# Kernel optimization log

Measured on AMD Instinct MI355X. Metric: run time of the kernel, lower is better.

## Reference

```python
import jax, jax.numpy as jnp
import numpy as np

B, T, D, H = 2, 4096, 768, 12
DK = D // H

def setup_inputs() -> dict:
    key = jax.random.key(0)
    ks = jax.random.split(key, 5)
    scale = 1.0 / np.sqrt(D)
    x = jax.random.normal(ks[0], (B, T, D), dtype=jnp.float32)
    WQ = jax.random.normal(ks[1], (D, D), dtype=jnp.float32) * scale
    WK = jax.random.normal(ks[2], (D, D), dtype=jnp.float32) * scale
    WV = jax.random.normal(ks[3], (D, D), dtype=jnp.float32) * scale
    Wproj = jax.random.normal(ks[4], (D, D), dtype=jnp.float32) * scale
    return {"x": x, "WQ": WQ, "WK": WK, "WV": WV, "Wproj": Wproj}

def reference(x, WQ, WK, WV, Wproj):
    # Weights stored as [in, out] (torch Linear weight transposed): y = x @ W
    def split_heads(y):
        return y.reshape(B, T, H, DK).transpose(0, 2, 1, 3)  # [B,H,T,DK]
    Q = split_heads(x @ WQ)
    K = split_heads(x @ WK)
    V = split_heads(x @ WV)
    score = jnp.einsum('bhqd,bhkd->bhqk', Q, K) * (DK ** -0.5)  # [B,H,T,T]
    attn = jax.nn.softmax(score, axis=-1)
    out = jnp.einsum('bhqk,bhkd->bhqd', attn, V)  # [B,H,T,DK]
    out = out.transpose(0, 2, 1, 3).reshape(B, T, D)
    return out @ Wproj
```

## Files before the change

kernel.cpp:

```cpp
#include <hip/hip_runtime.h>
#include <stdint.h>

#define B_ 2
#define T_ 4096
#define D_ 768
#define H_ 12
#define DK_ 64
#define BH_ 24

typedef unsigned short u16;
typedef unsigned int u32;
typedef __bf16 bf16x8 __attribute__((ext_vector_type(8)));
typedef float f32x4 __attribute__((ext_vector_type(4)));
typedef short s16x8 __attribute__((ext_vector_type(8)));

__device__ __forceinline__ float exp2_raw(float x) {
#if __has_builtin(__builtin_amdgcn_exp2f)
    return __builtin_amdgcn_exp2f(x);
#else
    float y; asm("v_exp_f32 %0, %1" : "=v"(y) : "v"(x)); return y;
#endif
}

__device__ __forceinline__ f32x4 mfma16(bf16x8 a, bf16x8 b, f32x4 c) {
    return __builtin_amdgcn_mfma_f32_16x16x32_bf16(a, b, c, 0, 0, 0);
}

__device__ __forceinline__ u16 f2bf(float f) {
    union { float f; u32 u; } v; v.f = f;
    u32 r = v.u + 0x7FFFu + ((v.u >> 16) & 1u);
    return (u16)(r >> 16);
}

__device__ __forceinline__ u32 pack2bf(float lo, float hi) {
    union { float f; u32 u; } a, b; a.f = lo; b.f = hi;
    return __builtin_amdgcn_perm(b.u + 0x8000u, a.u + 0x8000u, 0x07060302u);
}

__device__ __forceinline__ void gll16(const u16* g, u16* l) {
    __builtin_amdgcn_global_load_lds(
        (const __attribute__((address_space(1))) u32*)g,
        (__attribute__((address_space(3))) u32*)l, 16, 0, 0);
}

__global__ __launch_bounds__(256) void prep_kernel(
    const float* __restrict__ x,
    const float* __restrict__ w0, const float* __restrict__ w1,
    const float* __restrict__ w2, const float* __restrict__ w3,
    u16* __restrict__ xb, u16* __restrict__ wt)
{
    __shared__ u16 tile[32][33];
    int bid = blockIdx.x;
    if (bid < 3072) {
        int i = (bid * 256 + threadIdx.x) * 8;
        float4 a = *(const float4*)&x[i];
        float4 b = *(const float4*)&x[i + 4];
        uint4 dd;
        dd.x = pack2bf(a.x, a.y); dd.y = pack2bf(a.z, a.w);
        dd.z = pack2bf(b.x, b.y); dd.w = pack2bf(b.z, b.w);
        *(uint4*)&xb[i] = dd;
    } else {
        int id = bid - 3072;
        int z = id / 576;
        int rest = id % 576;
        int by = rest / 24, bx = rest % 24;
        const float* src = (z == 0) ? w0 : (z == 1) ? w1 : (z == 2) ? w2 : w3;
        u16* dst = wt + (size_t)z * D_ * D_;
        int tx = threadIdx.x & 31, ty = threadIdx.x >> 5;
        int x0 = bx * 32, y0 = by * 32;
        for (int i = ty; i < 32; i += 8) tile[i][tx] = f2bf(src[(size_t)(y0 + i) * D_ + x0 + tx]);
        __syncthreads();
        for (int i = ty; i < 32; i += 8) dst[(size_t)(x0 + i) * D_ + y0 + tx] = tile[tx][i];
    }
}

template<int MODE>
__global__ __launch_bounds__(256) void gemm_bt(
    const u16* __restrict__ A, const u16* __restrict__ Bt, void* __restrict__ outv)
{
    __shared__ u16 As[128 * 64];
    __shared__ u16 Bs[128 * 64];
    const int K = 768;
    int tid = threadIdx.x;
    int lane = tid & 63, wave = tid >> 6;
    int r = lane & 15, quad = lane >> 4;
    int rx = r & 7;
    int m0 = blockIdx.y * 128, n0 = blockIdx.x * 128;
    int wrow = (wave >> 1) * 64, wcol = (wave & 1) * 64;

    int srow = wave * 32 + (lane >> 3);
    int scol = ((lane & 7) ^ (lane >> 3)) * 8;
    const u16* Ag = A + (size_t)(m0 + srow) * K + scol;
    const u16* Bg = Bt + (size_t)(n0 + srow) * K + scol;

    f32x4 acc[4][4];
    #pragma unroll
    for (int i = 0; i < 4; i++)
        #pragma unroll
        for (int j = 0; j < 4; j++)
            #pragma unroll
            for (int e = 0; e < 4; e++) acc[i][j][e] = 0.f;

    for (int k0 = 0; k0 < K; k0 += 64) {
        __syncthreads();
        #pragma unroll
        for (int j = 0; j < 4; j++) {
            gll16(Ag + (size_t)j * 8 * K + k0, As + (wave * 32 + j * 8) * 64);
            gll16(Bg + (size_t)j * 8 * K + k0, Bs + (wave * 32 + j * 8) * 64);
        }
        __syncthreads();
        #pragma unroll
        for (int ks = 0; ks < 2; ks++) {
            int swz = ((ks * 4 + quad) ^ rx) * 8;
            bf16x8 af[4], bfr[4];
            #pragma unroll
            for (int mi = 0; mi < 4; mi++)
                af[mi] = *(const bf16x8*)&As[(wrow + mi * 16 + r) * 64 + swz];
            #pragma unroll
            for (int ni = 0; ni < 4; ni++)
                bfr[ni] = *(const bf16x8*)&Bs[(wcol + ni * 16 + r) * 64 + swz];
            #pragma unroll
            for (int mi = 0; mi < 4; mi++)
                #pragma unroll
                for (int ni = 0; ni < 4; ni++)
                    acc[mi][ni] = mfma16(af[mi], bfr[ni], acc[mi][ni]);
        }
    }

    if (MODE == 0) {
        u16* out = (u16*)outv;
        int which = n0 / D_;
        int nb = n0 % D_;
        const size_t HS = (size_t)B_ * H_ * T_ * DK_;
        if (which == 2) {
            u16* vt = out + 2 * HS;
            #pragma unroll
            for (int mi = 0; mi < 4; mi++) {
                int mg = m0 + wrow + mi * 16 + quad * 4;
                int b = mg >> 12, t = mg & 4095;
                #pragma unroll
                for (int ni = 0; ni < 4; ni++) {
                    int ng = nb + wcol + ni * 16 + r;
                    int h = ng >> 6, dk = ng & 63;
                    uint2 d;
                    d.x = pack2bf(acc[mi][ni][0], acc[mi][ni][1]);
                    d.y = pack2bf(acc[mi][ni][2], acc[mi][ni][3]);
                    *(uint2*)&vt[(((size_t)(b * H_ + h)) * DK_ + dk) * T_ + t] = d;
                }
            }
        } else {
            const float cf = (which == 0) ? 0.18033688011112042f : 1.0f;
            size_t wbase = (size_t)which * HS;
            #pragma unroll
            for (int mi = 0; mi < 4; mi++) {
                #pragma unroll
                for (int ni = 0; ni < 4; ni++) {
                    int ng = nb + wcol + ni * 16 + r;
                    int h = ng >> 6, dk = ng & 63;
                    #pragma unroll
                    for (int e = 0; e < 4; e++) {
                        int mg = m0 + wrow + mi * 16 + quad * 4 + e;
                        int b = mg >> 12, t = mg & 4095;
                        out[wbase + (((size_t)(b * H_ + h)) * T_ + t) * DK_ + dk]
                            = f2bf(acc[mi][ni][e] * cf);
                    }
                }
            }
        }
    } else {
        float* out = (float*)outv;
        #pragma unroll
        for (int mi = 0; mi < 4; mi++)
            #pragma unroll
            for (int ni = 0; ni < 4; ni++)
                #pragma unroll
                for (int e = 0; e < 4; e++)
                    out[(size_t)(m0 + wrow + mi * 16 + quad * 4 + e) * D_ + n0 + wcol + ni * 16 + r]
                        = acc[mi][ni][e];
    }
}

__global__ __launch_bounds__(512, 4) void attn_kernel(
    const u16* __restrict__ Q, const u16* __restrict__ K,
    const u16* __restrict__ VT, float* __restrict__ pO, float* __restrict__ pL)
{
    __shared__ u16 Ks[128 * 64];
    __shared__ u16 Vs[2][64 * 64];

    int tid = threadIdx.x;
    int lane = tid & 63, w = tid >> 6;
    int r = lane & 15, quad = lane >> 4;

    int wgid = blockIdx.x;
    int xcd = wgid & 7, slot = wgid >> 3;
    int bh = xcd * 3 + (slot >> 5);
    int rem = slot & 31;
    int z = rem >> 4;
    int q0 = (rem & 15) * 256;

    bf16x8 qf[2][2];
    #pragma unroll
    for (int qi = 0; qi < 2; qi++) {
        const u16* Qb = Q + ((size_t)bh * T_ + q0 + w * 32 + qi * 16 + r) * DK_;
        qf[qi][0] = *(const bf16x8*)(Qb + quad * 8);
        qf[qi][1] = *(const bf16x8*)(Qb + 32 + quad * 8);
    }

    bf16x8 ones;
    #pragma unroll
    for (int j = 0; j < 8; j++) ones[j] = (__bf16)1.0f;

    f32x4 fzero;
    #pragma unroll
    for (int e = 0; e < 4; e++) fzero[e] = 0.f;

    f32x4 o[2][4];
    f32x4 lacc[2];
    #pragma unroll
    for (int qi = 0; qi < 2; qi++) {
        #pragma unroll
        for (int e = 0; e < 4; e++) lacc[qi][e] = 0.f;
        #pragma unroll
        for (int n = 0; n < 4; n++)
            #pragma unroll
            for (int e = 0; e < 4; e++) o[qi][n][e] = 0.f;
    }

    int kb0 = z * (T_ / 2), kb1 = kb0 + T_ / 2;
    int rb = ((r >> 2) * 8) + (r & 3);

    int kls = lane >> 3;
    int sgcK1 = (lane & 7) ^ (kls & 3);
    const u16* KgA = K + ((size_t)bh * T_ + w * 16 + kls) * DK_ + sgcK1 * 8;
    const u16* KgB = K + ((size_t)bh * T_ + w * 16 + 8 + kls) * DK_ + (sgcK1 ^ 4) * 8;
    u16* KsA = &Ks[(w * 16) * 64];
    u16* KsB = &Ks[(w * 16 + 8) * 64];

    int srow = w * 8 + (lane >> 3);
    int sfr = (w & 1) * 4 + ((lane >> 3) & 3);
    int sgcV = (lane & 7) ^ sfr;
    const u16* Vg = VT + ((size_t)bh * DK_ + srow) * T_ + sgcV * 8;
    u16* Vs0Base = &Vs[0][(w * 8) * 64];
    u16* Vs1Base = &Vs[1][(w * 8) * 64];

    for (int kb = kb0; kb < kb1; kb += 128) {
        __syncthreads();
        gll16(KgA + (size_t)kb * DK_, KsA);
        gll16(KgB + (size_t)kb * DK_, KsB);
        gll16(Vg + kb, Vs0Base);
        gll16(Vg + kb + 64, Vs1Base);
        __syncthreads();

        #pragma unroll
        for (int s = 0; s < 4; s++) {
            int rowA = s * 32 + rb;
            int rowB = rowA + 4;
            int fA = ((rowA >> 3) & 1) * 4 + (rowA & 3);
            int fB = ((rowB >> 3) & 1) * 4 + (rowB & 3);
            bf16x8 kA0 = *(const bf16x8*)&Ks[rowA * 64 + (quad ^ fA) * 8];
            bf16x8 kA1 = *(const bf16x8*)&Ks[rowA * 64 + (((4 + quad) ^ fA)) * 8];
            bf16x8 kB0 = *(const bf16x8*)&Ks[rowB * 64 + (quad ^ fB) * 8];
            bf16x8 kB1 = *(const bf16x8*)&Ks[rowB * 64 + (((4 + quad) ^ fB)) * 8];
            const u16* Vsub = Vs[s >> 1];
            bf16x8 vf[4];
            #pragma unroll
            for (int ndk = 0; ndk < 4; ndk++) {
                int row = ndk * 16 + r;
                int fvr = ((row >> 3) & 1) * 4 + (row & 3);
                vf[ndk] = *(const bf16x8*)&Vsub[row * 64 + ((((s & 1) * 4 + quad) ^ fvr)) * 8];
            }
            #pragma unroll
            for (int qi = 0; qi < 2; qi++) {
                f32x4 zA, zB;
                zA = mfma16(kA0, qf[qi][0], fzero);
                zA = mfma16(kA1, qf[qi][1], zA);
                zB = mfma16(kB0, qf[qi][0], fzero);
                zB = mfma16(kB1, qf[qi][1], zB);
                bf16x8 pf;
                pf[0] = (__bf16)exp2_raw(zA[0]);
                pf[1] = (__bf16)exp2_raw(zA[1]);
                pf[2] = (__bf16)exp2_raw(zA[2]);
                pf[3] = (__bf16)exp2_raw(zA[3]);
                pf[4] = (__bf16)exp2_raw(zB[0]);
                pf[5] = (__bf16)exp2_raw(zB[1]);
                pf[6] = (__bf16)exp2_raw(zB[2]);
                pf[7] = (__bf16)exp2_raw(zB[3]);
                lacc[qi] = mfma16(ones, pf, lacc[qi]);
                #pragma unroll
                for (int ndk = 0; ndk < 4; ndk++)
                    o[qi][ndk] = mfma16(vf[ndk], pf, o[qi][ndk]);
            }
        }
    }

    const size_t SP = (size_t)BH_ * T_ * DK_;
    #pragma unroll
    for (int qi = 0; qi < 2; qi++) {
        int q = q0 + w * 32 + qi * 16 + r;
        float* base = pO + (size_t)z * SP + ((size_t)bh * T_ + q) * DK_;
        #pragma unroll
        for (int ndk = 0; ndk < 4; ndk++)
            *(f32x4*)&base[ndk * 16 + quad * 4] = o[qi][ndk];
    }
    if (quad == 0) {
        #pragma unroll
        for (int qi = 0; qi < 2; qi++)
            pL[(size_t)z * BH_ * T_ + (size_t)bh * T_ + q0 + w * 32 + qi * 16 + r]
                = lacc[qi][0];
    }
}

__global__ __launch_bounds__(256) void combine_kernel(
    const float* __restrict__ pO, const float* __restrict__ pL, u16* __restrict__ AO)
{
    const size_t SP = (size_t)BH_ * T_ * DK_;
    int bh = blockIdx.y;
    int b = bh / H_, h = bh % H_;
    int q = blockIdx.x * 64 + (threadIdx.x >> 2);
    int dk0 = (threadIdx.x & 3) * 16;
    size_t idx = ((size_t)bh * T_ + q) * DK_ + dk0;
    float l0 = pL[(size_t)bh * T_ + q];
    float l1 = pL[(size_t)BH_ * T_ + (size_t)bh * T_ + q];
    float inv = 1.0f / (l0 + l1);
    u16* dst = AO + ((size_t)b * T_ + q) * D_ + h * DK_ + dk0;
    #pragma unroll
    for (int i = 0; i < 2; i++) {
        float4 a0 = *(const float4*)&pO[idx + i * 8];
        float4 a1 = *(const float4*)&pO[idx + i * 8 + 4];
        float4 b0 = *(const float4*)&pO[SP + idx + i * 8];
        float4 b1 = *(const float4*)&pO[SP + idx + i * 8 + 4];
        uint4 dd;
        dd.x = pack2bf((a0.x + b0.x) * inv, (a0.y + b0.y) * inv);
        dd.y = pack2bf((a0.z + b0.z) * inv, (a0.w + b0.w) * inv);
        dd.z = pack2bf((a1.x + b1.x) * inv, (a1.y + b1.y) * inv);
        dd.w = pack2bf((a1.z + b1.z) * inv, (a1.w + b1.w) * inv);
        *(uint4*)&dst[i * 8] = dd;
    }
}

extern "C" void kernel_launch(void* const* d_in, const int* in_sizes, int n_in,
                              void* d_out, int out_size, void* d_ws, size_t ws_size,
                              hipStream_t stream)
{
    const float* x  = (const float*)d_in[0];
    const float* wq = (const float*)d_in[1];
    const float* wk = (const float*)d_in[2];
    const float* wv = (const float*)d_in[3];
    const float* wp = (const float*)d_in[4];

    u16* ws = (u16*)d_ws;
    const size_t XS = (size_t)B_ * T_ * D_;
    const size_t WT = (size_t)D_ * D_;
    const size_t HS = (size_t)B_ * H_ * T_ * DK_;
    u16* xb = ws;
    u16* wt = xb + XS;
    u16* q  = wt + 4 * WT;
    u16* k  = q + HS;
    u16* vt = k + HS;
    u16* ao = vt + HS;
    float* pL = (float*)(ao + HS);
    float* pO = pL + 2 * (size_t)BH_ * T_;

    prep_kernel<<<dim3(3072 + 2304), 256, 0, stream>>>(x, wq, wk, wv, wp, xb, wt);
    gemm_bt<0><<<dim3(18, 64), 256, 0, stream>>>(xb, wt, q);
    attn_kernel<<<dim3(768), 512, 0, stream>>>(q, k, vt, pO, pL);
    combine_kernel<<<dim3(64, 24), 256, 0, stream>>>(pO, pL, ao);
    gemm_bt<1><<<dim3(6, 64), 256, 0, stream>>>(ao, wt + 3 * WT, d_out);
}
```

Measured before the change: 257.2 us.

## Fuse split-KV combine into output projection GEMM A-tile loading

Removes the separate combine kernel. The output-projection GEMM now builds its A tile directly from the two fp32 partial attention outputs and their row sums, normalizes them, converts to bf16 and stores them into swizzled shared memory. This saves one launch plus the write and re-read of the bf16 attention-output buffer. In exchange, each of the 6 column blocks re-reads the fp32 partials, so that traffic is repeated sixfold. The A-side loads are also now synchronous global loads inside the K loop rather than async copies.

After: 284.9 us. 10.8% more time.

```diff
diff --git a/kernel.cpp b/kernel.cpp
--- a/kernel.cpp
+++ b/kernel.cpp
@@ -74,9 +74,8 @@
     }
 }
 
-template<int MODE>
 __global__ __launch_bounds__(256) void gemm_bt(
-    const u16* __restrict__ A, const u16* __restrict__ Bt, void* __restrict__ outv)
+    const u16* __restrict__ A, const u16* __restrict__ Bt, u16* __restrict__ out)
 {
     __shared__ u16 As[128 * 64];
     __shared__ u16 Bs[128 * 64];
@@ -127,8 +126,7 @@
         }
     }
 
-    if (MODE == 0) {
-        u16* out = (u16*)outv;
+    {
         int which = n0 / D_;
         int nb = n0 % D_;
         const size_t HS = (size_t)B_ * H_ * T_ * DK_;
@@ -167,17 +165,101 @@
                 }
             }
         }
-    } else {
-        float* out = (float*)outv;
-        #pragma unroll
-        for (int mi = 0; mi < 4; mi++)
+    }
+}
+
+__global__ __launch_bounds__(256) void gemm_combine(
+    const float* __restrict__ pO, const float* __restrict__ pL,
+    const u16* __restrict__ Bt, float* __restrict__ out)
+{
+    __shared__ u16 As[128 * 64];
+    __shared__ u16 Bs[128 * 64];
+    const int K = 768;
+    const size_t SP = (size_t)BH_ * T_ * DK_;
+    const size_t LP = (size_t)BH_ * T_;
+    int tid = threadIdx.x;
+    int lane = tid & 63, wave = tid >> 6;
+    int r = lane & 15, quad = lane >> 4;
+    int rx = r & 7;
+    int m0 = blockIdx.y * 128, n0 = blockIdx.x * 128;
+    int wrow = (wave >> 1) * 64, wcol = (wave & 1) * 64;
+
+    int srow = wave * 32 + (lane >> 3);
+    int scol = ((lane & 7) ^ (lane >> 3)) * 8;
+    const u16* Bg = Bt + (size_t)(n0 + srow) * K + scol;
+
+    size_t cO[4];
+    size_t cL[4];
+    #pragma unroll
+    for (int j = 0; j < 4; j++) {
+        int mg = m0 + srow + j * 8;
+        int b = mg >> 12, q = mg & 4095;
+        cO[j] = ((size_t)b * H_ * T_ + q) * DK_ + scol;
+        cL[j] = (size_t)b * H_ * T_ + q;
+    }
+    u16* AsW = As + (size_t)0;
+
+    f32x4 acc[4][4];
+    #pragma unroll
+    for (int i = 0; i < 4; i++)
+        #pragma unroll
+        for (int j = 0; j < 4; j++)
+            #pragma unroll
+            for (int e = 0; e < 4; e++) acc[i][j][e] = 0.f;
+
+    for (int k0 = 0; k0 < K; k0 += 64) {
+        int h = k0 >> 6;
+        size_t hO = (size_t)h * T_ * DK_;
+        size_t hL = (size_t)h * T_;
+        __syncthreads();
+        #pragma unroll
+        for (int j = 0; j < 4; j++)
+            gll16(Bg + (size_t)j * 8 * K + k0, Bs + (wave * 32 + j * 8) * 64);
+        #pragma unroll
+        for (int j = 0; j < 4; j++) {
+            float l0 = pL[cL[j] + hL];
+            float l1 = pL[LP + cL[j] + hL];
+            float inv = 1.0f / (l0 + l1);
+            const float* p0 = pO + cO[j] + hO;
+            const float* p1 = pO + SP + cO[j] + hO;
+            float4 a0 = *(const float4*)&p0[0];
+            float4 a1 = *(const float4*)&p0[4];
+            float4 b0 = *(const float4*)&p1[0];
+            float4 b1 = *(const float4*)&p1[4];
+            uint4 dd;
+            dd.x = pack2bf((a0.x + b0.x) * inv, (a0.y + b0.y) * inv);
+            dd.y = pack2bf((a0.z + b0.z) * inv, (a0.w + b0.w) * inv);
+            dd.z = pack2bf((a1.x + b1.x) * inv, (a1.y + b1.y) * inv);
+            dd.w = pack2bf((a1.z + b1.z) * inv, (a1.w + b1.w) * inv);
+            *(uint4*)&AsW[(wave * 32 + j * 8) * 64 + lane * 8] = dd;
+        }
+        __syncthreads();
+        #pragma unroll
+        for (int ks = 0; ks < 2; ks++) {
+            int swz = ((ks * 4 + quad) ^ rx) * 8;
+            bf16x8 af[4], bfr[4];
+            #pragma unroll
+            for (int mi = 0; mi < 4; mi++)
+                af[mi] = *(const bf16x8*)&As[(wrow + mi * 16 + r) * 64 + swz];
             #pragma unroll
             for (int ni = 0; ni < 4; ni++)
+                bfr[ni] = *(const bf16x8*)&Bs[(wcol + ni * 16 + r) * 64 + swz];
+            #pragma unroll
+            for (int mi = 0; mi < 4; mi++)
                 #pragma unroll
-                for (int e = 0; e < 4; e++)
-                    out[(size_t)(m0 + wrow + mi * 16 + quad * 4 + e) * D_ + n0 + wcol + ni * 16 + r]
-                        = acc[mi][ni][e];
-    }
+                for (int ni = 0; ni < 4; ni++)
+                    acc[mi][ni] = mfma16(af[mi], bfr[ni], acc[mi][ni]);
+        }
+    }
+
+    #pragma unroll
+    for (int mi = 0; mi < 4; mi++)
+        #pragma unroll
+        for (int ni = 0; ni < 4; ni++)
+            #pragma unroll
+            for (int e = 0; e < 4; e++)
+                out[(size_t)(m0 + wrow + mi * 16 + quad * 4 + e) * D_ + n0 + wcol + ni * 16 + r]
+                    = acc[mi][ni][e];
 }
 
 __global__ __launch_bounds__(512, 4) void attn_kernel(
@@ -310,34 +392,6 @@
     }
 }
 
-__global__ __launch_bounds__(256) void combine_kernel(
-    const float* __restrict__ pO, const float* __restrict__ pL, u16* __restrict__ AO)
-{
-    const size_t SP = (size_t)BH_ * T_ * DK_;
-    int bh = blockIdx.y;
-    int b = bh / H_, h = bh % H_;
-    int q = blockIdx.x * 64 + (threadIdx.x >> 2);
-    int dk0 = (threadIdx.x & 3) * 16;
-    size_t idx = ((size_t)bh * T_ + q) * DK_ + dk0;
-    float l0 = pL[(size_t)bh * T_ + q];
-    float l1 = pL[(size_t)BH_ * T_ + (size_t)bh * T_ + q];
-    float inv = 1.0f / (l0 + l1);
-    u16* dst = AO + ((size_t)b * T_ + q) * D_ + h * DK_ + dk0;
-    #pragma unroll
-    for (int i = 0; i < 2; i++) {
-        float4 a0 = *(const float4*)&pO[idx + i * 8];
-        float4 a1 = *(const float4*)&pO[idx + i * 8 + 4];
-        float4 b0 = *(const float4*)&pO[SP + idx + i * 8];
-        float4 b1 = *(const float4*)&pO[SP + idx + i * 8 + 4];
-        uint4 dd;
-        dd.x = pack2bf((a0.x + b0.x) * inv, (a0.y + b0.y) * inv);
-        dd.y = pack2bf((a0.z + b0.z) * inv, (a0.w + b0.w) * inv);
-        dd.z = pack2bf((a1.x + b1.x) * inv, (a1.y + b1.y) * inv);
-        dd.w = pack2bf((a1.z + b1.z) * inv, (a1.w + b1.w) * inv);
-        *(uint4*)&dst[i * 8] = dd;
-    }
-}
-
 extern "C" void kernel_launch(void* const* d_in, const int* in_sizes, int n_in,
                               void* d_out, int out_size, void* d_ws, size_t ws_size,
                               hipStream_t stream)
@@ -362,8 +416,7 @@
     float* pO = pL + 2 * (size_t)BH_ * T_;
 
     prep_kernel<<<dim3(3072 + 2304), 256, 0, stream>>>(x, wq, wk, wv, wp, xb, wt);
-    gemm_bt<0><<<dim3(18, 64), 256, 0, stream>>>(xb, wt, q);
+    gemm_bt<<<dim3(18, 64), 256, 0, stream>>>(xb, wt, q);
     attn_kernel<<<dim3(768), 512, 0, stream>>>(q, k, vt, pO, pL);
-    combine_kernel<<<dim3(64, 24), 256, 0, stream>>>(pO, pL, ao);
-    gemm_bt<1><<<dim3(6, 64), 256, 0, stream>>>(ao, wt + 3 * WT, d_out);
-}
+    gemm_combine<<<dim3(6, 64), 256, 0, stream>>>(pO, pL, wt + 3 * WT, (float*)d_out);
+}
```

## Double-buffer K/V shared-memory tiles in attention loop to overlap loads with compute

Applied to the files above, without the earlier changes.

The attention kernel now keeps two shared-memory copies of the K and V tiles. It issues the async global-to-LDS loads for the next 128-key tile before computing on the current one, and needs one barrier per tile instead of two. The aim is to hide global load latency behind the MFMA and exp work. In exchange, per-block LDS grows from 32KB to 64KB, which may cut the number of resident blocks per CU below the launch-bounds target of 4.

Result: no change. 254.3 us (-1.1%).

```diff
diff --git a/kernel.cpp b/kernel.cpp
--- a/kernel.cpp
+++ b/kernel.cpp
@@ -184,8 +184,8 @@
     const u16* __restrict__ Q, const u16* __restrict__ K,
     const u16* __restrict__ VT, float* __restrict__ pO, float* __restrict__ pL)
 {
-    __shared__ u16 Ks[128 * 64];
-    __shared__ u16 Vs[2][64 * 64];
+    __shared__ u16 Ks[2][128 * 64];
+    __shared__ u16 Vs[2][2][64 * 64];
 
     int tid = threadIdx.x;
     int lane = tid & 63, w = tid >> 6;
@@ -233,35 +233,40 @@
     int sgcK1 = (lane & 7) ^ (kls & 3);
     const u16* KgA = K + ((size_t)bh * T_ + w * 16 + kls) * DK_ + sgcK1 * 8;
     const u16* KgB = K + ((size_t)bh * T_ + w * 16 + 8 + kls) * DK_ + (sgcK1 ^ 4) * 8;
-    u16* KsA = &Ks[(w * 16) * 64];
-    u16* KsB = &Ks[(w * 16 + 8) * 64];
 
     int srow = w * 8 + (lane >> 3);
     int sfr = (w & 1) * 4 + ((lane >> 3) & 3);
     int sgcV = (lane & 7) ^ sfr;
     const u16* Vg = VT + ((size_t)bh * DK_ + srow) * T_ + sgcV * 8;
-    u16* Vs0Base = &Vs[0][(w * 8) * 64];
-    u16* Vs1Base = &Vs[1][(w * 8) * 64];
-
-    for (int kb = kb0; kb < kb1; kb += 128) {
-        __syncthreads();
-        gll16(KgA + (size_t)kb * DK_, KsA);
-        gll16(KgB + (size_t)kb * DK_, KsB);
-        gll16(Vg + kb, Vs0Base);
-        gll16(Vg + kb + 64, Vs1Base);
-        __syncthreads();
-
+
+    u16* KsA0 = &Ks[0][(w * 16) * 64];
+    u16* KsB0 = &Ks[0][(w * 16 + 8) * 64];
+    u16* KsA1 = &Ks[1][(w * 16) * 64];
+    u16* KsB1 = &Ks[1][(w * 16 + 8) * 64];
+    u16* V00 = &Vs[0][0][(w * 8) * 64];
+    u16* V01 = &Vs[0][1][(w * 8) * 64];
+    u16* V10 = &Vs[1][0][(w * 8) * 64];
+    u16* V11 = &Vs[1][1][(w * 8) * 64];
+
+    auto stage_tile = [&](int kb, u16* ksA, u16* ksB, u16* vs0, u16* vs1) {
+        gll16(KgA + (size_t)kb * DK_, ksA);
+        gll16(KgB + (size_t)kb * DK_, ksB);
+        gll16(Vg + kb, vs0);
+        gll16(Vg + kb + 64, vs1);
+    };
+
+    auto compute_tile = [&](const u16* Kc, const u16* V0, const u16* V1) {
         #pragma unroll
         for (int s = 0; s < 4; s++) {
             int rowA = s * 32 + rb;
             int rowB = rowA + 4;
             int fA = ((rowA >> 3) & 1) * 4 + (rowA & 3);
             int fB = ((rowB >> 3) & 1) * 4 + (rowB & 3);
-            bf16x8 kA0 = *(const bf16x8*)&Ks[rowA * 64 + (quad ^ fA) * 8];
-            bf16x8 kA1 = *(const bf16x8*)&Ks[rowA * 64 + (((4 + quad) ^ fA)) * 8];
-            bf16x8 kB0 = *(const bf16x8*)&Ks[rowB * 64 + (quad ^ fB) * 8];
-            bf16x8 kB1 = *(const bf16x8*)&Ks[rowB * 64 + (((4 + quad) ^ fB)) * 8];
-            const u16* Vsub = Vs[s >> 1];
+            bf16x8 kA0 = *(const bf16x8*)&Kc[rowA * 64 + (quad ^ fA) * 8];
+            bf16x8 kA1 = *(const bf16x8*)&Kc[rowA * 64 + (((4 + quad) ^ fA)) * 8];
+            bf16x8 kB0 = *(const bf16x8*)&Kc[rowB * 64 + (quad ^ fB) * 8];
+            bf16x8 kB1 = *(const bf16x8*)&Kc[rowB * 64 + (((4 + quad) ^ fB)) * 8];
+            const u16* Vsub = (s < 2) ? V0 : V1;
             bf16x8 vf[4];
             #pragma unroll
             for (int ndk = 0; ndk < 4; ndk++) {
@@ -291,6 +296,19 @@
                     o[qi][ndk] = mfma16(vf[ndk], pf, o[qi][ndk]);
             }
         }
+    };
+
+    stage_tile(kb0, KsA0, KsB0, V00, V01);
+    __syncthreads();
+
+    for (int kb = kb0; kb < kb1; kb += 256) {
+        stage_tile(kb + 128, KsA1, KsB1, V10, V11);
+        compute_tile(Ks[0], Vs[0][0], Vs[0][1]);
+        __syncthreads();
+        if (kb + 256 < kb1)
+            stage_tile(kb + 256, KsA0, KsB0, V00, V01);
+        compute_tile(Ks[1], Vs[1][0], Vs[1][1]);
+        __syncthreads();
     }
 
     const size_t SP = (size_t)BH_ * T_ * DK_;
```
